# Optimization experiments

Hardware: AMD Instinct MI355X
Metric: run time of the kernel (lower is better)

## Reference

```python
import jax, jax.numpy as jnp
import numpy as np
import math

B, S, D, H, R = 4, 4096, 1024, 16, 256
DK = D // H

def setup_inputs() -> dict:
    key = jax.random.key(0)
    ks = jax.random.split(key, 16)
    def lin(k, fan_in, fan_out):
        # torch Linear default init: U(-1/sqrt(fan_in), 1/sqrt(fan_in))
        bound = 1.0 / math.sqrt(fan_in)
        kw, kb = jax.random.split(k)
        W = jax.random.uniform(kw, (fan_out, fan_in), jnp.float32, -bound, bound)
        b = jax.random.uniform(kb, (fan_out,), jnp.float32, -bound, bound)
        return W, b
    Wq, bq = lin(ks[0], D, D)
    Wk, bk = lin(ks[1], D, D)
    Wv, bv = lin(ks[2], D, D)
    Wo, bo = lin(ks[3], D, D)
    # xavier_uniform over last two dims (S, R)
    xav = math.sqrt(6.0 / (S + R))
    E = jax.random.uniform(ks[4], (H, S, R), jnp.float32, -xav, xav)
    F = jax.random.uniform(ks[5], (H, S, R), jnp.float32, -xav, xav)
    query = jax.random.normal(ks[6], (B, S, D), jnp.float32)
    key_ = jax.random.normal(ks[7], (B, S, D), jnp.float32)
    value = jax.random.normal(ks[8], (B, S, D), jnp.float32)
    return {"query": query, "key": key_, "value": value,
            "Wq": Wq, "bq": bq, "Wk": Wk, "bk": bk, "Wv": Wv, "bv": bv,
            "Wo": Wo, "bo": bo, "E": E, "F": F}

def _split_heads(x):
    # [B, S, D] -> [B, H, S, DK]
    b, s, _ = x.shape
    return x.reshape(b, s, H, DK).transpose(0, 2, 1, 3)

def reference(query, key, value, Wq, bq, Wk, bk, Wv, bv, Wo, bo, E, F):
    q = _split_heads(query @ Wq.T + bq)   # [B,H,S,DK]
    k = _split_heads(key @ Wk.T + bk)
    v = _split_heads(value @ Wv.T + bv)
    # key^T @ E : [B,H,DK,S] @ [H,S,R] -> [B,H,DK,R]
    kp = jnp.einsum('bhsd,hsr->bhdr', k, E)
    vp = jnp.einsum('bhsd,hsr->bhdr', v, F)
    attn = jnp.einsum('bhsd,bhdr->bhsr', q, kp) / math.sqrt(DK)
    attn = jax.nn.softmax(attn, axis=-1)  # [B,H,S,R]
    out = jnp.einsum('bhsr,bhdr->bhsd', attn, vp)  # [B,H,S,DK]
    out = out.transpose(0, 2, 1, 3).reshape(query.shape[0], -1, D)
    return out @ Wo.T + bo
```

## Files before the change

### kernel.cpp

```cpp
#include <hip/hip_runtime.h>


typedef __bf16 bf16;
typedef bf16 bf16x8 __attribute__((ext_vector_type(8)));
typedef bf16 bf16x4 __attribute__((ext_vector_type(4)));
typedef float f32x4 __attribute__((ext_vector_type(4)));

constexpr int BB = 4, SS = 4096, DD = 1024, HH = 16, RR = 256, DK = 64;

#define QSCALE 0.1803368801111204f

__device__ __forceinline__ void gl2lds16(const void* g, void* l, int lane)
{
#if __has_builtin(__builtin_amdgcn_global_load_lds)
    auto gp = reinterpret_cast<const __attribute__((address_space(1))) void*>(
        reinterpret_cast<uintptr_t>(g));
    auto lp = reinterpret_cast<__attribute__((address_space(3))) void*>(
        reinterpret_cast<uintptr_t>(l));
    __builtin_amdgcn_global_load_lds(gp, lp, 16, 0, 0);
    (void)lane;
#else
    *(bf16x8*)((char*)l + lane * 16) = *(const bf16x8*)g;
#endif
}

#define VMW4  asm volatile("s_waitcnt vmcnt(4)" ::: "memory")
#define VMW0  asm volatile("s_waitcnt vmcnt(0)" ::: "memory")
#define LGKM0 asm volatile("s_waitcnt lgkmcnt(0)" ::: "memory")

__global__ void cvt_f32_bf16(const float* __restrict__ in, bf16* __restrict__ out, int n)
{
    int i = (blockIdx.x * 256 + threadIdx.x) * 8;
    if (i < n) {
        float4 v0 = *(const float4*)(in + i);
        float4 v1 = *(const float4*)(in + i + 4);
        bf16x8 h;
        h[0] = (bf16)v0.x; h[1] = (bf16)v0.y; h[2] = (bf16)v0.z; h[3] = (bf16)v0.w;
        h[4] = (bf16)v1.x; h[5] = (bf16)v1.y; h[6] = (bf16)v1.z; h[7] = (bf16)v1.w;
        *(bf16x8*)(out + i) = h;
    }
}

__global__ void transpose_cvt(const float* __restrict__ in, bf16* __restrict__ out,
                              int rows, int cols)
{
    __shared__ float t[64][65];
    const float* I = in + (size_t)blockIdx.z * rows * cols;
    bf16* O = out + (size_t)blockIdx.z * rows * cols;
    int c0 = blockIdx.x * 64, r0 = blockIdx.y * 64;
    int tx = threadIdx.x, ty = threadIdx.y;
#pragma unroll
    for (int i = ty; i < 64; i += 4)
        t[i][tx] = I[(size_t)(r0 + i) * cols + c0 + tx];
    __syncthreads();
#pragma unroll
    for (int i = ty; i < 64; i += 4)
        O[(size_t)(c0 + i) * rows + r0 + tx] = (bf16)t[tx][i];
}

template <bool OUT_F32>
__global__ __launch_bounds__(512, 2) void gemm_bt(const bf16* __restrict__ A,
                                                  const bf16* __restrict__ W,
                                                  const float* __restrict__ bias,
                                                  void* __restrict__ Cp,
                                                  int M, int N, int K, float oscale)
{
    __shared__ bf16 As[2][256][64];
    __shared__ bf16 Bs[2][256][64];
    const int tid = threadIdx.x, wv = tid >> 6, lane = tid & 63;
    const int g = lane >> 4, lr = lane & 15;

    const int nwg = gridDim.x;
    const int cpx = nwg >> 3;
    const int bid = blockIdx.x;
    const int swz = (bid & 7) * cpx + (bid >> 3);
    const int gx = N >> 8;
    const int mt = swz / gx, nt = swz % gx;
    const int m0 = mt * 256, n0 = nt * 256;
    const int wm = (wv >> 2) * 128, wn = (wv & 3) * 64;

    const int lrow8 = lane >> 3;
    const int gcol = ((lane & 7) ^ lrow8) * 8;

    f32x4 acc[8][4] = {};

    auto stageA = [&](int buf, int tk, int h) {
#pragma unroll
        for (int s2 = 0; s2 < 2; ++s2) {
            int j = wv + s2 * 8;
            int rb = h * 64 + (j >> 3) * 128 + (j & 7) * 8;
            gl2lds16(A + (size_t)(m0 + rb + lrow8) * 1024 + tk * 64 + gcol,
                     &As[buf][rb][0], lane);
        }
    };
    auto stageB = [&](int buf, int tk, int h) {
#pragma unroll
        for (int s2 = 0; s2 < 2; ++s2) {
            int j = wv + s2 * 8;
            int rb = h * 32 + (j >> 2) * 64 + (j & 3) * 8;
            gl2lds16(W + (size_t)(n0 + rb + lrow8) * 1024 + tk * 64 + gcol,
                     &Bs[buf][rb][0], lane);
        }
    };

#define PHASE(PB, MH, NH, STAGE_STMT, VM_STMT)                                   \
    {                                                                            \
        bf16x8 aF[4][2], bF[2][2];                                               \
        _Pragma("unroll") for (int m = 0; m < 4; ++m) {                          \
            _Pragma("unroll") for (int kk = 0; kk < 2; ++kk) {                   \
                aF[m][kk] = *(const bf16x8*)((const char*)&As[PB][wm + MH * 64 + m * 16 + lr][0] \
                              + (((kk * 4 + g) ^ (lr & 7)) << 4)); } }           \
        _Pragma("unroll") for (int n = 0; n < 2; ++n) {                          \
            _Pragma("unroll") for (int kk = 0; kk < 2; ++kk) {                   \
                bF[n][kk] = *(const bf16x8*)((const char*)&Bs[PB][wn + NH * 32 + n * 16 + lr][0] \
                              + (((kk * 4 + g) ^ (lr & 7)) << 4)); } }           \
        STAGE_STMT;                                                              \
        VM_STMT;                                                                 \
        __builtin_amdgcn_s_barrier();                                            \
        LGKM0;                                                                   \
        __builtin_amdgcn_sched_barrier(0);                                       \
        __builtin_amdgcn_s_setprio(1);                                           \
        _Pragma("unroll") for (int kk = 0; kk < 2; ++kk) {                       \
            _Pragma("unroll") for (int m = 0; m < 4; ++m) {                      \
                _Pragma("unroll") for (int n = 0; n < 2; ++n) {                  \
                    acc[MH * 4 + m][NH * 2 + n] = __builtin_amdgcn_mfma_f32_16x16x32_bf16( \
                        aF[m][kk], bF[n][kk], acc[MH * 4 + m][NH * 2 + n], 0, 0, 0); } } } \
        __builtin_amdgcn_s_setprio(0);                                           \
        __builtin_amdgcn_s_barrier();                                            \
    }

    stageA(0, 0, 0); stageB(0, 0, 0); stageA(0, 0, 1); stageB(0, 0, 1);
    stageA(1, 1, 0); stageB(1, 1, 0);
    VMW4;
    __builtin_amdgcn_s_barrier();

#pragma unroll 1
    for (int t = 0; t < 14; t += 2) {
        PHASE(0, 0, 0, stageA(1, t + 1, 1), (void)0);
        PHASE(0, 0, 1, stageB(1, t + 1, 1), (void)0);
        PHASE(0, 1, 0, stageA(0, t + 2, 0), (void)0);
        PHASE(0, 1, 1, stageB(0, t + 2, 0), VMW4);
        PHASE(1, 0, 0, stageA(0, t + 2, 1), (void)0);
        PHASE(1, 0, 1, stageB(0, t + 2, 1), (void)0);
        PHASE(1, 1, 0, stageA(1, t + 3, 0), (void)0);
        PHASE(1, 1, 1, stageB(1, t + 3, 0), VMW4);
    }
    PHASE(0, 0, 0, stageA(1, 15, 1), (void)0);
    PHASE(0, 0, 1, stageB(1, 15, 1), (void)0);
    PHASE(0, 1, 0, (void)0, (void)0);
    PHASE(0, 1, 1, (void)0, VMW0);
    PHASE(1, 0, 0, (void)0, (void)0);
    PHASE(1, 0, 1, (void)0, (void)0);
    PHASE(1, 1, 0, (void)0, (void)0);
    PHASE(1, 1, 1, (void)0, (void)0);
#undef PHASE

    float bv[4];
#pragma unroll
    for (int n = 0; n < 4; ++n) bv[n] = bias[n0 + wn + n * 16 + lr];

    if constexpr (OUT_F32) {
#pragma unroll
        for (int n = 0; n < 4; ++n) {
            int col = n0 + wn + n * 16 + lr;
#pragma unroll
            for (int m = 0; m < 8; ++m) {
                int row = m0 + wm + m * 16 + 4 * g;
#pragma unroll
                for (int i = 0; i < 4; ++i)
                    ((float*)Cp)[(size_t)(row + i) * N + col] = (acc[m][n][i] + bv[n]) * oscale;
            }
        }
    } else {
        bf16* myb = (wv < 4) ? (&As[0][0][0] + wv * 8192)
                             : (&Bs[0][0][0] + (wv - 4) * 8192);
#pragma unroll
        for (int m = 0; m < 8; ++m)
#pragma unroll
            for (int n = 0; n < 4; ++n) {
                int colb = n * 32 + lr * 2;
#pragma unroll
                for (int i = 0; i < 4; ++i) {
                    int row = m * 16 + 4 * g + i;
                    *(bf16*)((char*)myb + row * 128 + (colb ^ ((row & 7) << 4))) =
                        (bf16)((acc[m][n][i] + bv[n]) * oscale);
                }
            }
        __builtin_amdgcn_wave_barrier();
        bf16* Cb = (bf16*)Cp + (size_t)(m0 + wm) * N + n0 + wn;
#pragma unroll
        for (int it = 0; it < 16; ++it) {
            int r = it * 8 + lrow8;
            int sl = lane & 7;
            bf16x8 vv = *(const bf16x8*)((const char*)myb + r * 128 + ((sl ^ (r & 7)) << 4));
            *(bf16x8*)(Cb + (size_t)r * N + sl * 8) = vv;
        }
    }
}

__global__ __launch_bounds__(256) void kpvp_gemm(const bf16* __restrict__ X,
                                                 const bf16* __restrict__ P,
                                                 float* __restrict__ out)
{
    __shared__ bf16 Ak[64][40];
    __shared__ bf16 Bs[256][32];
    const int b = blockIdx.z, h = blockIdx.y;
    const int s0 = blockIdx.x * 512;
    const int tid = threadIdx.x, wv = tid >> 6, lane = tid & 63;
    const int g = lane >> 4, lr = lane & 15;
    const int lrow = lane >> 2, lcol = (lane & 3) * 8;
    const bf16* Pg = P + ((size_t)h * RR + wv * 64 + lrow) * SS + lcol;
    f32x4 acc[4][4] = {};

    for (int kt = 0; kt < 512; kt += 32) {
        const int sb = s0 + kt;
        __syncthreads();
#pragma unroll
        for (int j = 0; j < 4; ++j)
            gl2lds16(Pg + (size_t)(j * 16) * SS + sb, &Bs[wv * 64 + j * 16][0], lane);
        {
            int sl = tid >> 3, dblk = (tid & 7) * 8;
            bf16x8 v = *(const bf16x8*)(X + ((size_t)b * SS + sb + sl) * DD + h * DK + dblk);
#pragma unroll
            for (int j = 0; j < 8; ++j) Ak[dblk + j][sl] = v[j];
        }
        __syncthreads();

        bf16x8 a[4], bb[4];
#pragma unroll
        for (int m = 0; m < 4; ++m) a[m] = *(const bf16x8*)&Ak[m * 16 + lr][g * 8];
#pragma unroll
        for (int n = 0; n < 4; ++n) bb[n] = *(const bf16x8*)&Bs[wv * 64 + n * 16 + lr][g * 8];
#pragma unroll
        for (int m = 0; m < 4; ++m)
#pragma unroll
            for (int n = 0; n < 4; ++n)
                acc[m][n] = __builtin_amdgcn_mfma_f32_16x16x32_bf16(a[m], bb[n], acc[m][n], 0, 0, 0);
    }

    float* o = out + ((size_t)(b * HH + h)) * DK * RR;
#pragma unroll
    for (int m = 0; m < 4; ++m)
#pragma unroll
        for (int n = 0; n < 4; ++n) {
            int r = wv * 64 + n * 16 + lr;
#pragma unroll
            for (int i = 0; i < 4; ++i)
                atomicAdd(o + (size_t)(m * 16 + 4 * g + i) * RR + r, acc[m][n][i]);
        }
}

__global__ __launch_bounds__(512) void attn_fused(const bf16* __restrict__ qb,
                                                  const bf16* __restrict__ kpt,
                                                  const bf16* __restrict__ vpb,
                                                  bf16* __restrict__ ctx)
{
    __shared__ bf16 KPs[256][72];
    __shared__ bf16 VPs[64][264];
    __shared__ bf16 Ps[8][16][264];
    const int b = blockIdx.z, h = blockIdx.y, qt = blockIdx.x;
    const int tid = threadIdx.x, wv = tid >> 6, lane = tid & 63;
    const int g = lane >> 4, lr = lane & 15;
    const bf16* kph = kpt + ((size_t)(b * HH + h)) * RR * DK;
    const bf16* vph = vpb + ((size_t)(b * HH + h)) * DK * RR;

#pragma unroll
    for (int p = 0; p < 4; ++p) {
        int f = p * 512 + tid;
        *(bf16x8*)&KPs[f >> 3][(f & 7) * 8] = *(const bf16x8*)(kph + (size_t)f * 8);
        *(bf16x8*)&VPs[f >> 5][(f & 31) * 8] = *(const bf16x8*)(vph + (size_t)f * 8);
    }

    const bf16* qbase = qb + (size_t)b * SS * DD + h * DK;
    int row0 = qt * 1024 + wv * 16;
    bf16x8 aq0 = *(const bf16x8*)(qbase + (size_t)(row0 + lr) * DD + g * 8);
    bf16x8 aq1 = *(const bf16x8*)(qbase + (size_t)(row0 + lr) * DD + 32 + g * 8);
    __syncthreads();

    for (int it = 0; it < 8; ++it) {
        f32x4 acc[16] = {};
        __builtin_amdgcn_s_setprio(1);
#pragma unroll
        for (int nf = 0; nf < 16; ++nf) {
            bf16x8 b0 = *(const bf16x8*)&KPs[nf * 16 + lr][g * 8];
            bf16x8 b1 = *(const bf16x8*)&KPs[nf * 16 + lr][32 + g * 8];
            acc[nf] = __builtin_amdgcn_mfma_f32_16x16x32_bf16(aq0, b0, acc[nf], 0, 0, 0);
            acc[nf] = __builtin_amdgcn_mfma_f32_16x16x32_bf16(aq1, b1, acc[nf], 0, 0, 0);
        }
        __builtin_amdgcn_s_setprio(0);

        bf16x8 aqn0 = aq0, aqn1 = aq1;
        if (it < 7) {
            const bf16* qr = qbase + (size_t)(row0 + 128 + lr) * DD;
            aqn0 = *(const bf16x8*)(qr + g * 8);
            aqn1 = *(const bf16x8*)(qr + 32 + g * 8);
        }

        float rs[4];
#pragma unroll
        for (int i = 0; i < 4; ++i) {
            float s = 0.f;
#pragma unroll
            for (int nf = 0; nf < 16; ++nf) {
                float pv = exp2f(acc[nf][i]);
                acc[nf][i] = pv;
                s += pv;
            }
#pragma unroll
            for (int msk = 1; msk < 16; msk <<= 1) s += __shfl_xor(s, msk, 64);
            rs[i] = 1.f / s;
        }

#pragma unroll
        for (int nf = 0; nf < 16; ++nf)
#pragma unroll
            for (int i = 0; i < 4; ++i)
                Ps[wv][4 * g + i][nf * 16 + lr] = (bf16)acc[nf][i];
        __builtin_amdgcn_wave_barrier();

        f32x4 o[4] = {};
        __builtin_amdgcn_s_setprio(1);
#pragma unroll
        for (int ks = 0; ks < 8; ++ks) {
            bf16x8 pa = *(const bf16x8*)&Ps[wv][lr][ks * 32 + g * 8];
#pragma unroll
            for (int n = 0; n < 4; ++n) {
                bf16x8 vb = *(const bf16x8*)&VPs[n * 16 + lr][ks * 32 + g * 8];
                o[n] = __builtin_amdgcn_mfma_f32_16x16x32_bf16(pa, vb, o[n], 0, 0, 0);
            }
        }
        __builtin_amdgcn_s_setprio(0);
        __builtin_amdgcn_wave_barrier();

#pragma unroll
        for (int n = 0; n < 4; ++n)
#pragma unroll
            for (int i = 0; i < 4; ++i)
                Ps[wv][4 * g + i][n * 16 + lr] = (bf16)(o[n][i] * rs[i]);
        __builtin_amdgcn_wave_barrier();
        bf16* crow = ctx + (size_t)(b * SS + row0) * DD + h * DK;
#pragma unroll
        for (int p = 0; p < 2; ++p) {
            int r = p * 8 + (lane >> 3), c = (lane & 7) * 8;
            bf16x8 ov = *(const bf16x8*)&Ps[wv][r][c];
            *(bf16x8*)(crow + (size_t)r * DD + c) = ov;
        }
        __builtin_amdgcn_wave_barrier();

        aq0 = aqn0; aq1 = aqn1;
        row0 += 128;
    }
}

extern "C" void kernel_launch(void* const* d_in, const int* in_sizes, int n_in,
                              void* d_out, int out_size, void* d_ws, size_t ws_size,
                              hipStream_t stream)
{
    const float* query = (const float*)d_in[0];
    const float* key   = (const float*)d_in[1];
    const float* value = (const float*)d_in[2];
    const float* Wq = (const float*)d_in[3];  const float* bq = (const float*)d_in[4];
    const float* Wk = (const float*)d_in[5];  const float* bk = (const float*)d_in[6];
    const float* Wv = (const float*)d_in[7];  const float* bv = (const float*)d_in[8];
    const float* Wo = (const float*)d_in[9];  const float* bo = (const float*)d_in[10];
    const float* E  = (const float*)d_in[11];
    const float* F  = (const float*)d_in[12];

    char* w = (char*)d_ws;
    size_t off = 0;
    auto alloc = [&](size_t bytes) -> char* {
        char* p = w + off;
        off += (bytes + 255) & ~(size_t)255;
        return p;
    };

    const size_t DW   = (size_t)DD * DD;
    const size_t BSD  = (size_t)BB * SS * DD;
    const size_t HRS  = (size_t)HH * RR * SS;
    const size_t BHDR = (size_t)BB * HH * DK * RR;

    bf16* wqb = (bf16*)alloc(DW * 2);
    bf16* wkb = (bf16*)alloc(DW * 2);
    bf16* wvb = (bf16*)alloc(DW * 2);
    bf16* wob = (bf16*)alloc(DW * 2);
    bf16* ebt = (bf16*)alloc(HRS * 2);
    bf16* fbt = (bf16*)alloc(HRS * 2);
    bf16* qin = (bf16*)alloc(BSD * 2);
    bf16* kin = (bf16*)alloc(BSD * 2);
    bf16* vin = (bf16*)alloc(BSD * 2);
    bf16* qbuf = (bf16*)alloc(BSD * 2);
    bf16* kbuf = (bf16*)alloc(BSD * 2);
    bf16* vbuf = (bf16*)alloc(BSD * 2);
    if (off > ws_size) return;

    float* kpf  = (float*)qin;
    float* vpf  = kpf + BHDR;
    bf16*  kpt  = (bf16*)kin;
    bf16*  vpbb = kpt + BHDR;
    bf16*  ctx  = (bf16*)vin;

    cvt_f32_bf16<<<(int)(DW / 2048), 256, 0, stream>>>(Wq, wqb, (int)DW);
    cvt_f32_bf16<<<(int)(DW / 2048), 256, 0, stream>>>(Wk, wkb, (int)DW);
    cvt_f32_bf16<<<(int)(DW / 2048), 256, 0, stream>>>(Wv, wvb, (int)DW);
    cvt_f32_bf16<<<(int)(DW / 2048), 256, 0, stream>>>(Wo, wob, (int)DW);
    cvt_f32_bf16<<<(int)(BSD / 2048), 256, 0, stream>>>(query, qin, (int)BSD);
    cvt_f32_bf16<<<(int)(BSD / 2048), 256, 0, stream>>>(key,   kin, (int)BSD);
    cvt_f32_bf16<<<(int)(BSD / 2048), 256, 0, stream>>>(value, vin, (int)BSD);

    dim3 tb(64, 4);
    transpose_cvt<<<dim3(RR / 64, SS / 64, HH), tb, 0, stream>>>(E, ebt, SS, RR);
    transpose_cvt<<<dim3(RR / 64, SS / 64, HH), tb, 0, stream>>>(F, fbt, SS, RR);

    const int nwg = ((BB * SS) / 256) * (DD / 256);
    gemm_bt<false><<<nwg, 512, 0, stream>>>(qin, wqb, bq, qbuf, BB * SS, DD, DD, QSCALE);
    gemm_bt<false><<<nwg, 512, 0, stream>>>(kin, wkb, bk, kbuf, BB * SS, DD, DD, 1.0f);
    gemm_bt<false><<<nwg, 512, 0, stream>>>(vin, wvb, bv, vbuf, BB * SS, DD, DD, 1.0f);

    hipMemsetAsync(kpf, 0, BHDR * 4 * 2, stream);
    kpvp_gemm<<<dim3(SS / 512, HH, BB), 256, 0, stream>>>(kbuf, ebt, kpf);
    kpvp_gemm<<<dim3(SS / 512, HH, BB), 256, 0, stream>>>(vbuf, fbt, vpf);

    transpose_cvt<<<dim3(RR / 64, DK / 64, BB * HH), tb, 0, stream>>>(kpf, kpt, DK, RR);
    cvt_f32_bf16<<<(int)(BHDR / 2048), 256, 0, stream>>>(vpf, vpbb, (int)BHDR);

    attn_fused<<<dim3(SS / 1024, HH, BB), 512, 0, stream>>>(qbuf, kpt, vpbb, ctx);

    gemm_bt<true><<<nwg, 512, 0, stream>>>(ctx, wob, bo, d_out, BB * SS, DD, DD, 1.0f);
}
```

Measured before the change: 434.8 us.

## Restructure GEMM mainloop to four phases reusing full B fragments per k-tile

The GEMM mainloop now runs four phases per k-tile instead of eight. B fragments for all four n-subtiles are loaded once per buffer and kept in registers across both M halves, so each phase issues 32 MFMAs and the redundant B LDS reads go away. The global-to-LDS staging order and the vmcnt wait thresholds are rearranged to match, with two loads per phase and a wait of two outstanding. The cost is more live VGPRs for the persistent B fragments, which could lower occupancy, and only half as many barrier-separated phases to hide load latency.

```diff
diff --git a/kernel.cpp b/kernel.cpp
--- a/kernel.cpp
+++ b/kernel.cpp
@@ -24,7 +24,7 @@
 #endif
 }
 
-#define VMW4  asm volatile("s_waitcnt vmcnt(4)" ::: "memory")
+#define VMW2  asm volatile("s_waitcnt vmcnt(2)" ::: "memory")
 #define VMW0  asm volatile("s_waitcnt vmcnt(0)" ::: "memory")
 #define LGKM0 asm volatile("s_waitcnt lgkmcnt(0)" ::: "memory")
 
@@ -83,6 +83,7 @@
     const int gcol = ((lane & 7) ^ lrow8) * 8;
 
     f32x4 acc[8][4] = {};
+    bf16x8 bF[4][2];
 
     auto stageA = [&](int buf, int tk, int h) {
 #pragma unroll
@@ -103,17 +104,19 @@
         }
     };
 
-#define PHASE(PB, MH, NH, STAGE_STMT, VM_STMT)                                   \
+#define PH(PB, MH, LOADB, STAGE_STMT, VM_STMT)                                   \
     {                                                                            \
-        bf16x8 aF[4][2], bF[2][2];                                               \
-        _Pragma("unroll") for (int m = 0; m < 4; ++m) {                          \
+        bf16x8 aF[4][2];                                                         \
+        _Pragma("unroll") for (int mm = 0; mm < 4; ++mm) {                       \
             _Pragma("unroll") for (int kk = 0; kk < 2; ++kk) {                   \
-                aF[m][kk] = *(const bf16x8*)((const char*)&As[PB][wm + MH * 64 + m * 16 + lr][0] \
+                aF[mm][kk] = *(const bf16x8*)((const char*)&As[PB][wm + MH * 64 + mm * 16 + lr][0] \
                               + (((kk * 4 + g) ^ (lr & 7)) << 4)); } }           \
-        _Pragma("unroll") for (int n = 0; n < 2; ++n) {                          \
-            _Pragma("unroll") for (int kk = 0; kk < 2; ++kk) {                   \
-                bF[n][kk] = *(const bf16x8*)((const char*)&Bs[PB][wn + NH * 32 + n * 16 + lr][0] \
-                              + (((kk * 4 + g) ^ (lr & 7)) << 4)); } }           \
+        if (LOADB) {                                                             \
+            _Pragma("unroll") for (int j = 0; j < 4; ++j) {                      \
+                _Pragma("unroll") for (int kk = 0; kk < 2; ++kk) {               \
+                    bF[j][kk] = *(const bf16x8*)((const char*)&Bs[PB][wn + j * 16 + lr][0] \
+                                  + (((kk * 4 + g) ^ (lr & 7)) << 4)); } }       \
+        }                                                                        \
         STAGE_STMT;                                                              \
         VM_STMT;                                                                 \
         __builtin_amdgcn_s_barrier();                                            \
@@ -121,39 +124,31 @@
         __builtin_amdgcn_sched_barrier(0);                                       \
         __builtin_amdgcn_s_setprio(1);                                           \
         _Pragma("unroll") for (int kk = 0; kk < 2; ++kk) {                       \
-            _Pragma("unroll") for (int m = 0; m < 4; ++m) {                      \
-                _Pragma("unroll") for (int n = 0; n < 2; ++n) {                  \
-                    acc[MH * 4 + m][NH * 2 + n] = __builtin_amdgcn_mfma_f32_16x16x32_bf16( \
-                        aF[m][kk], bF[n][kk], acc[MH * 4 + m][NH * 2 + n], 0, 0, 0); } } } \
+            _Pragma("unroll") for (int mm = 0; mm < 4; ++mm) {                   \
+                _Pragma("unroll") for (int j = 0; j < 4; ++j) {                  \
+                    acc[MH * 4 + mm][j] = __builtin_amdgcn_mfma_f32_16x16x32_bf16( \
+                        aF[mm][kk], bF[j][kk], acc[MH * 4 + mm][j], 0, 0, 0); } } } \
         __builtin_amdgcn_s_setprio(0);                                           \
         __builtin_amdgcn_s_barrier();                                            \
     }
 
-    stageA(0, 0, 0); stageB(0, 0, 0); stageA(0, 0, 1); stageB(0, 0, 1);
-    stageA(1, 1, 0); stageB(1, 1, 0);
-    VMW4;
+    stageA(0, 0, 0); stageA(0, 0, 1); stageB(0, 0, 0); stageB(0, 0, 1);
+    stageA(1, 1, 0);
+    VMW2;
     __builtin_amdgcn_s_barrier();
 
 #pragma unroll 1
-    for (int t = 0; t < 14; t += 2) {
-        PHASE(0, 0, 0, stageA(1, t + 1, 1), (void)0);
-        PHASE(0, 0, 1, stageB(1, t + 1, 1), (void)0);
-        PHASE(0, 1, 0, stageA(0, t + 2, 0), (void)0);
-        PHASE(0, 1, 1, stageB(0, t + 2, 0), VMW4);
-        PHASE(1, 0, 0, stageA(0, t + 2, 1), (void)0);
-        PHASE(1, 0, 1, stageB(0, t + 2, 1), (void)0);
-        PHASE(1, 1, 0, stageA(1, t + 3, 0), (void)0);
-        PHASE(1, 1, 1, stageB(1, t + 3, 0), VMW4);
-    }
-    PHASE(0, 0, 0, stageA(1, 15, 1), (void)0);
-    PHASE(0, 0, 1, stageB(1, 15, 1), (void)0);
-    PHASE(0, 1, 0, (void)0, (void)0);
-    PHASE(0, 1, 1, (void)0, VMW0);
-    PHASE(1, 0, 0, (void)0, (void)0);
-    PHASE(1, 0, 1, (void)0, (void)0);
-    PHASE(1, 1, 0, (void)0, (void)0);
-    PHASE(1, 1, 1, (void)0, (void)0);
-#undef PHASE
+    for (int t = 0; t < 13; t += 2) {
+        PH(0, 0, true,  { stageB(1, t + 1, 0); stageB(1, t + 1, 1); }, (void)0);
+        PH(0, 1, false, { stageA(1, t + 1, 1); stageA(0, t + 2, 0); }, VMW2);
+        PH(1, 0, true,  { stageA(0, t + 2, 1); stageB(0, t + 2, 0); }, (void)0);
+        PH(1, 1, false, { stageB(0, t + 2, 1); stageA(1, t + 3, 0); }, VMW2);
+    }
+    PH(0, 0, true,  { stageB(1, 15, 0); stageB(1, 15, 1); }, (void)0);
+    PH(0, 1, false, { stageA(1, 15, 1); }, VMW0);
+    PH(1, 0, true,  (void)0, (void)0);
+    PH(1, 1, false, (void)0, (void)0);
+#undef PH
 
     float bv[4];
 #pragma unroll
```

Result: slower. 458.2 us (+5.4%).
